# Performance work log

Measured on AMD Instinct MI355X. Metric: run time of the kernel, lower is better.

Reference implementation:

```python
import jax, jax.numpy as jnp
import numpy as np

B, T, C, H, HS, L, V = 16, 2048, 16, 2, 8, 2, 256
EPS = 1e-5


def _ln(x, g, b):
    m = jnp.mean(x, axis=-1, keepdims=True)
    v = jnp.mean((x - m) ** 2, axis=-1, keepdims=True)
    return (x - m) / jnp.sqrt(v + EPS) * g + b


def setup_inputs() -> dict:
    key = jax.random.key(0)
    ks = jax.random.split(key, 10)
    p = lambda k, s: (0.02 * jax.random.normal(k, s)).astype(jnp.float32)
    return {
        "idx": jax.random.randint(ks[0], (B, T), 0, V),
        "tok_emb": p(ks[1], (V, C)),          # tied with lm_head
        "pos_emb": p(ks[2], (T, C)),
        "wq": p(ks[3], (L, H, C, HS)),
        "wk": p(ks[4], (L, H, C, HS)),
        "wv": p(ks[5], (L, H, C, HS)),
        "wo": p(ks[6], (L, C, C)),            # torch Linear weight: (out, in)
        "ln1_g": jnp.ones((L, C), jnp.float32),
        "ln1_b": jnp.zeros((L, C), jnp.float32),
        "ln2_g": jnp.ones((L, C), jnp.float32),
        "ln2_b": jnp.zeros((L, C), jnp.float32),
        "w1": p(ks[7], (L, 4 * C, C)),
        "w2": p(ks[8], (L, C, 4 * C)),
        "lnf_g": jnp.ones((C,), jnp.float32),
        "lnf_b": jnp.zeros((C,), jnp.float32),
    }


def reference(idx, tok_emb, pos_emb, wq, wk, wv, wo, ln1_g, ln1_b,
              ln2_g, ln2_b, w1, w2, lnf_g, lnf_b):
    Tc = idx.shape[1]
    x = tok_emb[idx] + pos_emb[:Tc]                      # [B,T,C]
    causal = jnp.tril(jnp.ones((Tc, Tc), dtype=bool))
    scale = HS ** -0.5
    for l in range(L):
        h = _ln(x, ln1_g[l], ln1_b[l])
        q = jnp.einsum('btc,hcs->bhts', h, wq[l])
        k = jnp.einsum('btc,hcs->bhts', h, wk[l])
        v = jnp.einsum('btc,hcs->bhts', h, wv[l])
        scores = jnp.einsum('bhts,bhus->bhtu', q, k) * scale
        scores = jnp.where(causal, scores, -jnp.inf)
        attn = jax.nn.softmax(scores, axis=-1)           # [B,H,T,T]
        o = jnp.einsum('bhtu,bhus->bhts', attn, v)       # [B,H,T,HS]
        o = o.transpose(0, 2, 1, 3).reshape(x.shape[0], Tc, C)  # concat heads
        x = x + o @ wo[l].T
        h = _ln(x, ln2_g[l], ln2_b[l])
        x = x + jax.nn.relu(h @ w1[l].T) @ w2[l].T
    x = _ln(x, lnf_g, lnf_b)
    return x @ tok_emb.T                                 # tied lm_head: [B,T,V]
```

## Files before the change

kernel.cpp:

```cpp
#include <hip/hip_runtime.h>
#include <math.h>

constexpr int Bc  = 16;
constexpr int Tc  = 2048;
constexpr int Cc  = 16;
constexpr int Hc  = 2;
constexpr int HSc = 8;
constexpr int Vc  = 256;
constexpr int BT  = Bc * Tc;
constexpr float EPSc = 1e-5f;


typedef short s8v __attribute__((ext_vector_type(8)));
typedef float f4v __attribute__((ext_vector_type(4)));

__device__ inline float shx(float v, int m) { return __shfl_xor(v, m, 64); }

__device__ inline unsigned short f2bf(float f) {
  union { float f; unsigned u; } c; c.f = f;
  unsigned u = c.u + 0x7fffu + ((c.u >> 16) & 1u);
  return (unsigned short)(u >> 16);
}

__device__ inline unsigned cvtpk(float a, float b) {
  unsigned r;
  asm("v_cvt_pk_bf16_f32 %0, %1, %2" : "=v"(r) : "v"(a), "v"(b));
  return r;
}

__device__ inline void layernorm16(const float* xr, float* h,
                                   const float* g, const float* b) {
  float m = 0.f;
#pragma unroll
  for (int c = 0; c < Cc; c++) m += xr[c];
  m *= (1.f / Cc);
  float var = 0.f;
#pragma unroll
  for (int c = 0; c < Cc; c++) { float d = xr[c] - m; var += d * d; }
  var *= (1.f / Cc);
  float rs = rsqrtf(var + EPSc);
#pragma unroll
  for (int c = 0; c < Cc; c++) h[c] = (xr[c] - m) * rs * g[c] + b[c];
}

__device__ inline void qkv_store_bf16(const float* h, const float* swq,
                                      const float* swk, const float* swv,
                                      int bb, int tt, int j,
                                      unsigned short* __restrict__ qb,
                                      unsigned short* __restrict__ kb,
                                      unsigned short* sv) {
  const float pre = 0.35355339059327373f * 1.4426950408889634f;
  int a = tt & 31;
  int col = (tt & 32) | ((((a & 15) >> 2)) << 3) | (((a >> 4) & 1) << 2) |
            (a & 3);
#pragma unroll
  for (int hh = 0; hh < Hc; hh++) {
    float q0 = 0.f, q1 = 0.f, k0 = 0.f, k1 = 0.f, v0 = 0.f, v1 = 0.f;
#pragma unroll
    for (int c = 0; c < Cc; c++) {
      float hv = h[c];
      const float* wqp = swq + (hh * Cc + c) * HSc + 2 * j;
      const float* wkp = swk + (hh * Cc + c) * HSc + 2 * j;
      const float* wvp = swv + (hh * Cc + c) * HSc + 2 * j;
      q0 += hv * wqp[0]; q1 += hv * wqp[1];
      k0 += hv * wkp[0]; k1 += hv * wkp[1];
      v0 += hv * wvp[0]; v1 += hv * wvp[1];
    }
    int bh = bb * Hc + hh;
    long rowb = ((long)bh * Tc + tt) * 8 + 2 * j;
    unsigned qp = (unsigned)f2bf(q0 * pre) | ((unsigned)f2bf(q1 * pre) << 16);
    unsigned kp = (unsigned)f2bf(k0) | ((unsigned)f2bf(k1) << 16);
    *(unsigned*)(qb + rowb) = qp;
    *(unsigned*)(kb + rowb) = kp;
    sv[(hh * 8 + 2 * j) * 64 + col]     = f2bf(v0);
    sv[(hh * 8 + 2 * j + 1) * 64 + col] = f2bf(v1);
  }
}

__device__ inline void vt_writeout(const unsigned short* sv, int bb, int t0,
                                   int tid, unsigned short* __restrict__ vt) {
  int r  = tid >> 4;
  int cs = (tid & 15) * 4;
  int bh = bb * Hc + (r >> 3);
  int d  = r & 7;
  *(uint2*)(vt + ((long)bh * 8 + d) * Tc + t0 + cs) =
      *(const uint2*)(sv + r * 64 + cs);
}

__global__ __launch_bounds__(256, 4) void embed_ln_qkv_kernel(
    const int* __restrict__ idx, const float* __restrict__ tok,
    const float* __restrict__ pos,
    const float* __restrict__ wq, const float* __restrict__ wk,
    const float* __restrict__ wv,
    const float* __restrict__ g, const float* __restrict__ b,
    float* __restrict__ x, unsigned short* __restrict__ qb,
    unsigned short* __restrict__ kb, unsigned short* __restrict__ vt,
    unsigned short* __restrict__ zp, unsigned short* __restrict__ tokb) {
  __shared__ float swq[256], swk[256], swv[256], sg[Cc], sb[Cc];
  __shared__ unsigned short sv[16 * 64];
  int tid = threadIdx.x;
  if (blockIdx.x == 0) {
    if (tid < 16) ((unsigned*)zp)[tid] = 0u;
    const float4* tp = (const float4*)(tok + tid * Cc);
    float4 t0 = tp[0], t1 = tp[1], t2 = tp[2], t3 = tp[3];
    unsigned* tb = (unsigned*)(tokb + tid * 16);
    tb[0] = cvtpk(t0.x, t0.y); tb[1] = cvtpk(t0.z, t0.w);
    tb[2] = cvtpk(t1.x, t1.y); tb[3] = cvtpk(t1.z, t1.w);
    tb[4] = cvtpk(t2.x, t2.y); tb[5] = cvtpk(t2.z, t2.w);
    tb[6] = cvtpk(t3.x, t3.y); tb[7] = cvtpk(t3.z, t3.w);
  }
  swq[tid] = wq[tid];
  swk[tid] = wk[tid];
  swv[tid] = wv[tid];
  if (tid < Cc) { sg[tid] = g[tid]; sb[tid] = b[tid]; }
  __syncthreads();

  int tk = blockIdx.x * 64 + (tid >> 2);
  int j  = tid & 3;
  int tt = tk & (Tc - 1);
  int bb = tk >> 11;
  int id = idx[tk];
  float xr[Cc];
  const float4* te = (const float4*)(tok + id * Cc);
  const float4* pe = (const float4*)(pos + tt * Cc);
#pragma unroll
  for (int i = 0; i < 4; i++) {
    float4 a = te[i], p = pe[i];
    xr[4*i] = a.x + p.x; xr[4*i+1] = a.y + p.y;
    xr[4*i+2] = a.z + p.z; xr[4*i+3] = a.w + p.w;
  }
  ((float4*)(x + (long)tk * Cc))[j] =
      make_float4(xr[4*j], xr[4*j+1], xr[4*j+2], xr[4*j+3]);
  float h[Cc];
  layernorm16(xr, h, sg, sb);
  qkv_store_bf16(h, swq, swk, swv, bb, tt, j, qb, kb, sv);
  __syncthreads();
  vt_writeout(sv, bb, (blockIdx.x * 64) & (Tc - 1), tid, vt);
}

__global__ __launch_bounds__(64, 4) void attn_kernel(
    const unsigned short* __restrict__ qb,
    const unsigned short* __restrict__ kb,
    const unsigned short* __restrict__ vt,
    const unsigned short* __restrict__ zp,
    float* __restrict__ o) {
  int pairId = blockIdx.x >> 5;
  int bh     = blockIdx.x & 31;
  int lane   = threadIdx.x;
  int lq     = lane & 15;
  int g4     = (lane >> 4) << 2;
  bool real16 = lane < 16;
  bool real8  = lq < 8;
  bool md[4];
#pragma unroll
  for (int r = 0; r < 4; r++) md[r] = (g4 + r) <= lq;

  const f4v zf = {0.f, 0.f, 0.f, 0.f};

#pragma unroll 1
  for (int hf = 0; hf < 2; hf++) {
    int qt = hf ? (127 - pairId) : pairId;
    int q0 = qt << 4;
    int NB = (qt + 2) >> 1;

    s8v qf = *(real16 ? (const s8v*)(qb + ((long)bh * Tc + q0 + lq) * 8)
                      : (const s8v*)zp);
    const unsigned short* kp_ = real16 ? kb + ((long)bh * Tc + lq) * 8
                                       : zp;
    long kts = real16 ? 128 : 0;
    const unsigned short* vp_ =
        real8 ? vt + ((long)bh * 8 + lq) * Tc + (g4 << 1) : zp;
    long vts = real8 ? 32 : 0;

    f4v oacc = zf;
    float lsum = 0.f;

    s8v kf0 = *(const s8v*)kp_;
    s8v kf1 = *(const s8v*)(kp_ + kts);
    kp_ += 2 * kts;
    s8v vf = *(const s8v*)vp_;
    vp_ += vts;

    for (int b = 0; b < NB - 1; b++) {
      s8v kn0 = *(const s8v*)kp_;
      s8v kn1 = *(const s8v*)(kp_ + kts);
      kp_ += 2 * kts;
      s8v vn = *(const s8v*)vp_;
      vp_ += vts;

      f4v st0 = __builtin_amdgcn_mfma_f32_16x16x32_bf16(kf0, qf, zf, 0, 0, 0);
      f4v st1 = __builtin_amdgcn_mfma_f32_16x16x32_bf16(kf1, qf, zf, 0, 0, 0);
      float p00 = __builtin_amdgcn_exp2f(st0[0]);
      float p01 = __builtin_amdgcn_exp2f(st0[1]);
      float p02 = __builtin_amdgcn_exp2f(st0[2]);
      float p03 = __builtin_amdgcn_exp2f(st0[3]);
      float p10 = __builtin_amdgcn_exp2f(st1[0]);
      float p11 = __builtin_amdgcn_exp2f(st1[1]);
      float p12 = __builtin_amdgcn_exp2f(st1[2]);
      float p13 = __builtin_amdgcn_exp2f(st1[3]);
      lsum += ((p00 + p01) + (p02 + p03)) + ((p10 + p11) + (p12 + p13));
      union { unsigned u[4]; s8v s; } pu;
      pu.u[0] = cvtpk(p00, p01);
      pu.u[1] = cvtpk(p02, p03);
      pu.u[2] = cvtpk(p10, p11);
      pu.u[3] = cvtpk(p12, p13);
      oacc = __builtin_amdgcn_mfma_f32_16x16x32_bf16(pu.s, vf, oacc, 0, 0, 0);
      kf0 = kn0; kf1 = kn1; vf = vn;
    }

    {
      f4v st0 = __builtin_amdgcn_mfma_f32_16x16x32_bf16(kf0, qf, zf, 0, 0, 0);
      float p0[4], p1[4];
#pragma unroll
      for (int r = 0; r < 4; r++) p0[r] = __builtin_amdgcn_exp2f(st0[r]);
      if (qt & 1) {
        f4v st1 = __builtin_amdgcn_mfma_f32_16x16x32_bf16(kf1, qf, zf, 0, 0, 0);
#pragma unroll
        for (int r = 0; r < 4; r++) {
          float e = __builtin_amdgcn_exp2f(st1[r]);
          p1[r] = md[r] ? e : 0.f;
        }
      } else {
#pragma unroll
        for (int r = 0; r < 4; r++) {
          p0[r] = md[r] ? p0[r] : 0.f;
          p1[r] = 0.f;
        }
      }
      lsum += ((p0[0] + p0[1]) + (p0[2] + p0[3])) +
              ((p1[0] + p1[1]) + (p1[2] + p1[3]));
      union { unsigned u[4]; s8v s; } pu;
      pu.u[0] = cvtpk(p0[0], p0[1]);
      pu.u[1] = cvtpk(p0[2], p0[3]);
      pu.u[2] = cvtpk(p1[0], p1[1]);
      pu.u[3] = cvtpk(p1[2], p1[3]);
      oacc = __builtin_amdgcn_mfma_f32_16x16x32_bf16(pu.s, vf, oacc, 0, 0, 0);
    }

    lsum += shx(lsum, 16);
    lsum += shx(lsum, 32);
    float inv = 1.0f / lsum;
    float invr[4];
#pragma unroll
    for (int r = 0; r < 4; r++) invr[r] = __shfl(inv, g4 + r, 64);
    if (real8) {
      float* ob = o + ((long)bh * Tc + q0 + g4) * 8 + lq;
#pragma unroll
      for (int r = 0; r < 4; r++) ob[r * 8] = oacc[r] * invr[r];
    }
  }
}

__device__ inline void coop_tail(
    const float* __restrict__ o,
    const float* swo, const float* sw1, const float* sw2,
    const float* sg2, const float* sb2, int bb, int tt, int j, float* xr) {
  int hh = j & 1;
  int bh = bb * Hc + hh;
  const float4* op = (const float4*)(o + ((long)bh * Tc + tt) * 8);
  float4 a = op[0], b = op[1];
  float own[8] = {a.x, a.y, a.z, a.w, b.x, b.y, b.z, b.w};
  float oth[8];
#pragma unroll
  for (int s = 0; s < 8; s++) oth[s] = shx(own[s], 1);
  float orow[Cc];
#pragma unroll
  for (int s = 0; s < 8; s++) {
    orow[s]     = (hh == 0) ? own[s] : oth[s];
    orow[8 + s] = (hh == 0) ? oth[s] : own[s];
  }
  float xc[4];
#pragma unroll
  for (int qq = 0; qq < 4; qq++) {
    int c = 4 * j + qq;
    float acc = xr[c];
#pragma unroll
    for (int kk = 0; kk < Cc; kk++) acc += orow[kk] * swo[c * 17 + kk];
    xc[qq] = acc;
  }
  {
    float p[4];
#pragma unroll
    for (int qq = 0; qq < 4; qq++) p[qq] = shx(xc[qq], 1);
    bool lo = (j & 1) == 0;
    float a8[8], b8[8];
#pragma unroll
    for (int qq = 0; qq < 4; qq++) {
      a8[qq]     = lo ? xc[qq] : p[qq];
      a8[4 + qq] = lo ? p[qq] : xc[qq];
    }
#pragma unroll
    for (int s = 0; s < 8; s++) b8[s] = shx(a8[s], 2);
    bool lo2 = (j & 2) == 0;
#pragma unroll
    for (int s = 0; s < 8; s++) {
      xr[s]     = lo2 ? a8[s] : b8[s];
      xr[8 + s] = lo2 ? b8[s] : a8[s];
    }
  }
  float h[Cc];
  layernorm16(xr, h, sg2, sb2);
  float r[Cc];
#pragma unroll
  for (int c = 0; c < Cc; c++) r[c] = 0.f;
#pragma unroll
  for (int i = 0; i < 16; i++) {
    int jj = j * 16 + i;
    float acc = 0.f;
#pragma unroll
    for (int c = 0; c < Cc; c++) acc += h[c] * sw1[jj * 17 + c];
    acc = fmaxf(acc, 0.f);
#pragma unroll
    for (int c = 0; c < Cc; c++) r[c] += acc * sw2[c * 64 + jj];
  }
#pragma unroll
  for (int c = 0; c < Cc; c++) r[c] += shx(r[c], 1);
#pragma unroll
  for (int c = 0; c < Cc; c++) r[c] += shx(r[c], 2);
#pragma unroll
  for (int c = 0; c < Cc; c++) xr[c] += r[c];
}

__global__ __launch_bounds__(256, 4) void red_mid_kernel(
    const float* __restrict__ o,
    const float* __restrict__ wo, const float* __restrict__ g2,
    const float* __restrict__ b2, const float* __restrict__ w1,
    const float* __restrict__ w2,
    const float* __restrict__ wq, const float* __restrict__ wk,
    const float* __restrict__ wv, const float* __restrict__ g1,
    const float* __restrict__ b1,
    float* __restrict__ x, unsigned short* __restrict__ qb,
    unsigned short* __restrict__ kb, unsigned short* __restrict__ vt) {
  __shared__ float swo[16 * 17], sw1[64 * 17], sw2[1024];
  __shared__ float swq[256], swk[256], swv[256];
  __shared__ float sg2[Cc], sb2[Cc], sg1[Cc], sb1[Cc];
  __shared__ unsigned short sv[16 * 64];
  int tid = threadIdx.x;
  swq[tid] = wq[tid]; swk[tid] = wk[tid]; swv[tid] = wv[tid];
  { int rr = tid >> 4, c = tid & 15; swo[rr * 17 + c] = wo[tid]; }
#pragma unroll
  for (int t = tid; t < 1024; t += 256) {
    int jj = t >> 4, c = t & 15;
    sw1[jj * 17 + c] = w1[t];
    sw2[t] = w2[t];
  }
  if (tid < Cc) {
    sg2[tid] = g2[tid]; sb2[tid] = b2[tid];
    sg1[tid] = g1[tid]; sb1[tid] = b1[tid];
  }
  __syncthreads();

  int tk = blockIdx.x * 64 + (tid >> 2);
  int j  = tid & 3;
  int bb = tk >> 11, tt = tk & (Tc - 1);
  float xr[Cc];
  const float4* xp = (const float4*)(x + (long)tk * Cc);
#pragma unroll
  for (int i = 0; i < 4; i++) {
    float4 a = xp[i];
    xr[4*i]=a.x; xr[4*i+1]=a.y; xr[4*i+2]=a.z; xr[4*i+3]=a.w;
  }
  coop_tail(o, swo, sw1, sw2, sg2, sb2, bb, tt, j, xr);
  ((float4*)(x + (long)tk * Cc))[j] =
      make_float4(xr[4*j], xr[4*j+1], xr[4*j+2], xr[4*j+3]);
  float h[Cc];
  layernorm16(xr, h, sg1, sb1);
  qkv_store_bf16(h, swq, swk, swv, bb, tt, j, qb, kb, sv);
  __syncthreads();
  vt_writeout(sv, bb, (blockIdx.x * 64) & (Tc - 1), tid, vt);
}

__global__ __launch_bounds__(256, 4) void red_lnf_head_kernel(
    const float* __restrict__ o,
    const float* __restrict__ wo, const float* __restrict__ g2,
    const float* __restrict__ b2, const float* __restrict__ w1,
    const float* __restrict__ w2, const float* __restrict__ gf,
    const float* __restrict__ bf,
    const float* __restrict__ x, const unsigned short* __restrict__ tokb,
    const unsigned short* __restrict__ zp, float* __restrict__ out) {
  __shared__ float swo[16 * 17], sw1[64 * 17], sw2[1024];
  __shared__ float sg2[Cc], sb2[Cc], sgf[Cc], sbf[Cc];
  __shared__ unsigned short shb[64 * 16];
  int tid = threadIdx.x;
  { int rr = tid >> 4, c = tid & 15; swo[rr * 17 + c] = wo[tid]; }
#pragma unroll
  for (int t = tid; t < 1024; t += 256) {
    int jj = t >> 4, c = t & 15;
    sw1[jj * 17 + c] = w1[t];
    sw2[t] = w2[t];
  }
  if (tid < Cc) {
    sg2[tid] = g2[tid]; sb2[tid] = b2[tid];
    sgf[tid] = gf[tid]; sbf[tid] = bf[tid];
  }
  __syncthreads();

  int tk = blockIdx.x * 64 + (tid >> 2);
  int j  = tid & 3;
  int bb = tk >> 11, tt = tk & (Tc - 1);
  float xr[Cc];
  const float4* xp = (const float4*)(x + (long)tk * Cc);
#pragma unroll
  for (int i = 0; i < 4; i++) {
    float4 a = xp[i];
    xr[4*i]=a.x; xr[4*i+1]=a.y; xr[4*i+2]=a.z; xr[4*i+3]=a.w;
  }
  coop_tail(o, swo, sw1, sw2, sg2, sb2, bb, tt, j, xr);
  float h[Cc];
  layernorm16(xr, h, sgf, sbf);
  *(uint2*)(shb + (tid >> 2) * 16 + 4 * j) =
      make_uint2(cvtpk(h[4*j], h[4*j+1]), cvtpk(h[4*j+2], h[4*j+3]));
  __syncthreads();

  int wv = tid >> 6;
  int l  = tid & 63;
  int lg = l >> 4;
  bool realg = lg < 2;
  s8v hb = realg
      ? *(const s8v*)(shb + (wv * 16 + (l & 15)) * 16 + 8 * lg)
      : *(const s8v*)zp;
  const unsigned short* abase = realg ? tokb + (l & 15) * 16 + 8 * lg : zp;
  long astep = realg ? 256 : 0;
  const f4v zf = {0.f, 0.f, 0.f, 0.f};
  long trow = (long)(blockIdx.x * 64 + wv * 16 + (l & 15)) * Vc;
  int vbase = 4 * lg;
#pragma unroll 4
  for (int n = 0; n < 16; n++) {
    s8v af = *(const s8v*)(abase + n * astep);
    f4v d = __builtin_amdgcn_mfma_f32_16x16x32_bf16(af, hb, zf, 0, 0, 0);
    *(float4*)(out + trow + n * 16 + vbase) =
        make_float4(d[0], d[1], d[2], d[3]);
  }
}

extern "C" void kernel_launch(void* const* d_in, const int* in_sizes, int n_in,
                              void* d_out, int out_size, void* d_ws,
                              size_t ws_size, hipStream_t stream) {
  const int*   idx  = (const int*)  d_in[0];
  const float* tok  = (const float*)d_in[1];
  const float* pos  = (const float*)d_in[2];
  const float* wq   = (const float*)d_in[3];
  const float* wk   = (const float*)d_in[4];
  const float* wv   = (const float*)d_in[5];
  const float* wo   = (const float*)d_in[6];
  const float* ln1g = (const float*)d_in[7];
  const float* ln1b = (const float*)d_in[8];
  const float* ln2g = (const float*)d_in[9];
  const float* ln2b = (const float*)d_in[10];
  const float* w1   = (const float*)d_in[11];
  const float* w2   = (const float*)d_in[12];
  const float* lnfg = (const float*)d_in[13];
  const float* lnfb = (const float*)d_in[14];
  float* out = (float*)d_out;

  float* x = (float*)d_ws;
  float* o = x + (long)BT * Cc;
  unsigned short* qb = (unsigned short*)(o + (long)Bc * Hc * Tc * HSc);
  unsigned short* kb = qb + (long)Bc * Hc * Tc * HSc;
  unsigned short* vt = kb + (long)Bc * Hc * Tc * HSc;
  unsigned short* tokb = vt + (long)Bc * Hc * Tc * HSc;
  unsigned short* zp = tokb + Vc * Cc;

  embed_ln_qkv_kernel<<<BT / 64, 256, 0, stream>>>(
      idx, tok, pos, wq, wk, wv, ln1g, ln1b, x, qb, kb, vt, zp, tokb);
  attn_kernel<<<2048, 64, 0, stream>>>(qb, kb, vt, zp, o);
  red_mid_kernel<<<BT / 64, 256, 0, stream>>>(
      o, wo, ln2g, ln2b, w1, w2,
      wq + Hc * Cc * HSc, wk + Hc * Cc * HSc, wv + Hc * Cc * HSc,
      ln1g + Cc, ln1b + Cc, x, qb, kb, vt);
  attn_kernel<<<2048, 64, 0, stream>>>(qb, kb, vt, zp, o);
  red_lnf_head_kernel<<<BT / 64, 256, 0, stream>>>(
      o, wo + Cc * Cc, ln2g + Cc, ln2b + Cc,
      w1 + 4 * Cc * Cc, w2 + 4 * Cc * Cc, lnfg, lnfb, x, tokb, zp, out);
}
```

Baseline: 170.3 us.

## Fuse attention with the following MLP/QKV tail kernels via shared-memory handoff

Attention is now computed inside the per-layer tail kernel. Each 128-thread block handles both heads for one causal-balanced pair of query tiles and hands the attention output to the Wo/MLP/LN/QKV (or LN-final/lm_head) stage through shared memory instead of a global 'o' buffer. This removes two kernel launches and the global round trip of the attention output. Because the next layer's QKV is written while other blocks still read the current one, QKV/V^T buffers are double-buffered per layer. The trade-off is small 128-thread blocks that each reload all weights into LDS, and the attention phase's causal imbalance is now coupled with the tail work.

```diff
diff --git a/kernel.cpp b/kernel.cpp
--- a/kernel.cpp
+++ b/kernel.cpp
@@ -138,17 +138,14 @@
   vt_writeout(sv, bb, (blockIdx.x * 64) & (Tc - 1), tid, vt);
 }
 
-__global__ __launch_bounds__(64, 4) void attn_kernel(
-    const unsigned short* __restrict__ qb,
-    const unsigned short* __restrict__ kb,
-    const unsigned short* __restrict__ vt,
-    const unsigned short* __restrict__ zp,
-    float* __restrict__ o) {
-  int pairId = blockIdx.x >> 5;
-  int bh     = blockIdx.x & 31;
-  int lane   = threadIdx.x;
-  int lq     = lane & 15;
-  int g4     = (lane >> 4) << 2;
+__device__ inline void attn_wave(const unsigned short* __restrict__ qb,
+                                 const unsigned short* __restrict__ kb,
+                                 const unsigned short* __restrict__ vt,
+                                 const unsigned short* __restrict__ zp,
+                                 int bh, int pairId, int lane, int wv_,
+                                 float* so) {
+  int lq = lane & 15;
+  int g4 = (lane >> 4) << 2;
   bool real16 = lane < 16;
   bool real8  = lq < 8;
   bool md[4];
@@ -165,8 +162,7 @@
 
     s8v qf = *(real16 ? (const s8v*)(qb + ((long)bh * Tc + q0 + lq) * 8)
                       : (const s8v*)zp);
-    const unsigned short* kp_ = real16 ? kb + ((long)bh * Tc + lq) * 8
-                                       : zp;
+    const unsigned short* kp_ = real16 ? kb + ((long)bh * Tc + lq) * 8 : zp;
     long kts = real16 ? 128 : 0;
     const unsigned short* vp_ =
         real8 ? vt + ((long)bh * 8 + lq) * Tc + (g4 << 1) : zp;
@@ -214,7 +210,8 @@
 #pragma unroll
       for (int r = 0; r < 4; r++) p0[r] = __builtin_amdgcn_exp2f(st0[r]);
       if (qt & 1) {
-        f4v st1 = __builtin_amdgcn_mfma_f32_16x16x32_bf16(kf1, qf, zf, 0, 0, 0);
+        f4v st1 =
+            __builtin_amdgcn_mfma_f32_16x16x32_bf16(kf1, qf, zf, 0, 0, 0);
 #pragma unroll
         for (int r = 0; r < 4; r++) {
           float e = __builtin_amdgcn_exp2f(st1[r]);
@@ -244,30 +241,24 @@
 #pragma unroll
     for (int r = 0; r < 4; r++) invr[r] = __shfl(inv, g4 + r, 64);
     if (real8) {
-      float* ob = o + ((long)bh * Tc + q0 + g4) * 8 + lq;
-#pragma unroll
-      for (int r = 0; r < 4; r++) ob[r * 8] = oacc[r] * invr[r];
-    }
-  }
-}
-
-__device__ inline void coop_tail(
-    const float* __restrict__ o,
-    const float* swo, const float* sw1, const float* sw2,
-    const float* sg2, const float* sb2, int bb, int tt, int j, float* xr) {
-  int hh = j & 1;
-  int bh = bb * Hc + hh;
-  const float4* op = (const float4*)(o + ((long)bh * Tc + tt) * 8);
-  float4 a = op[0], b = op[1];
-  float own[8] = {a.x, a.y, a.z, a.w, b.x, b.y, b.z, b.w};
-  float oth[8];
-#pragma unroll
-  for (int s = 0; s < 8; s++) oth[s] = shx(own[s], 1);
+      float* ob = so + (hf * 16 + g4) * Cc + wv_ * 8 + lq;
+#pragma unroll
+      for (int r = 0; r < 4; r++) ob[r * Cc] = oacc[r] * invr[r];
+    }
+  }
+}
+
+__device__ inline void tail_core(
+    const float* so, const float* swo, const float* sw1, const float* sw2,
+    const float* sg2, const float* sb2, int tl, int j, float* xr) {
   float orow[Cc];
-#pragma unroll
-  for (int s = 0; s < 8; s++) {
-    orow[s]     = (hh == 0) ? own[s] : oth[s];
-    orow[8 + s] = (hh == 0) ? oth[s] : own[s];
+  {
+    const float4* op = (const float4*)(so + tl * Cc);
+    float4 a = op[0], b = op[1], c = op[2], d = op[3];
+    orow[0]=a.x; orow[1]=a.y; orow[2]=a.z; orow[3]=a.w;
+    orow[4]=b.x; orow[5]=b.y; orow[6]=b.z; orow[7]=b.w;
+    orow[8]=c.x; orow[9]=c.y; orow[10]=c.z; orow[11]=c.w;
+    orow[12]=d.x; orow[13]=d.y; orow[14]=d.z; orow[15]=d.w;
   }
   float xc[4];
 #pragma unroll
@@ -321,27 +312,31 @@
   for (int c = 0; c < Cc; c++) xr[c] += r[c];
 }
 
-__global__ __launch_bounds__(256, 4) void red_mid_kernel(
-    const float* __restrict__ o,
+__global__ __launch_bounds__(128, 2) void attn_mid_kernel(
+    const unsigned short* __restrict__ qb0,
+    const unsigned short* __restrict__ kb0,
+    const unsigned short* __restrict__ vt0,
+    const unsigned short* __restrict__ zp,
     const float* __restrict__ wo, const float* __restrict__ g2,
     const float* __restrict__ b2, const float* __restrict__ w1,
     const float* __restrict__ w2,
     const float* __restrict__ wq, const float* __restrict__ wk,
     const float* __restrict__ wv, const float* __restrict__ g1,
     const float* __restrict__ b1,
-    float* __restrict__ x, unsigned short* __restrict__ qb,
-    unsigned short* __restrict__ kb, unsigned short* __restrict__ vt) {
+    float* __restrict__ x, unsigned short* __restrict__ qb1,
+    unsigned short* __restrict__ kb1, unsigned short* __restrict__ vt1) {
   __shared__ float swo[16 * 17], sw1[64 * 17], sw2[1024];
   __shared__ float swq[256], swk[256], swv[256];
   __shared__ float sg2[Cc], sb2[Cc], sg1[Cc], sb1[Cc];
-  __shared__ unsigned short sv[16 * 64];
+  __shared__ float so[32 * Cc];
+  __shared__ unsigned short sv[2 * 16 * 16];
   int tid = threadIdx.x;
-  swq[tid] = wq[tid]; swk[tid] = wk[tid]; swv[tid] = wv[tid];
-  { int rr = tid >> 4, c = tid & 15; swo[rr * 17 + c] = wo[tid]; }
-#pragma unroll
-  for (int t = tid; t < 1024; t += 256) {
-    int jj = t >> 4, c = t & 15;
-    sw1[jj * 17 + c] = w1[t];
+  for (int t = tid; t < 256; t += 128) {
+    swq[t] = wq[t]; swk[t] = wk[t]; swv[t] = wv[t];
+    swo[(t >> 4) * 17 + (t & 15)] = wo[t];
+  }
+  for (int t = tid; t < 1024; t += 128) {
+    sw1[(t >> 4) * 17 + (t & 15)] = w1[t];
     sw2[t] = w2[t];
   }
   if (tid < Cc) {
@@ -350,43 +345,90 @@
   }
   __syncthreads();
 
-  int tk = blockIdx.x * 64 + (tid >> 2);
-  int j  = tid & 3;
-  int bb = tk >> 11, tt = tk & (Tc - 1);
+  int b  = blockIdx.x & 15;
+  int p  = blockIdx.x >> 4;
+  int wv_ = tid >> 6, lane = tid & 63;
+  attn_wave(qb0, kb0, vt0, zp, b * Hc + wv_, p, lane, wv_, so);
+  __syncthreads();
+
+  int tl = tid >> 2, j = tid & 3;
+  int qtT = (tl < 16) ? p : (127 - p);
+  int tt  = qtT * 16 + (tl & 15);
+  long tk = (long)b * Tc + tt;
   float xr[Cc];
-  const float4* xp = (const float4*)(x + (long)tk * Cc);
-#pragma unroll
-  for (int i = 0; i < 4; i++) {
-    float4 a = xp[i];
-    xr[4*i]=a.x; xr[4*i+1]=a.y; xr[4*i+2]=a.z; xr[4*i+3]=a.w;
-  }
-  coop_tail(o, swo, sw1, sw2, sg2, sb2, bb, tt, j, xr);
-  ((float4*)(x + (long)tk * Cc))[j] =
+  {
+    const float4* xp = (const float4*)(x + tk * Cc);
+#pragma unroll
+    for (int i = 0; i < 4; i++) {
+      float4 a = xp[i];
+      xr[4*i]=a.x; xr[4*i+1]=a.y; xr[4*i+2]=a.z; xr[4*i+3]=a.w;
+    }
+  }
+  tail_core(so, swo, sw1, sw2, sg2, sb2, tl, j, xr);
+  ((float4*)(x + tk * Cc))[j] =
       make_float4(xr[4*j], xr[4*j+1], xr[4*j+2], xr[4*j+3]);
   float h[Cc];
   layernorm16(xr, h, sg1, sb1);
-  qkv_store_bf16(h, swq, swk, swv, bb, tt, j, qb, kb, sv);
-  __syncthreads();
-  vt_writeout(sv, bb, (blockIdx.x * 64) & (Tc - 1), tid, vt);
-}
-
-__global__ __launch_bounds__(256, 4) void red_lnf_head_kernel(
-    const float* __restrict__ o,
+  {
+    const float pre = 0.35355339059327373f * 1.4426950408889634f;
+    int i  = tt & 15;
+    int cd = 4 * (i >> 2) + (i & 3);
+    int tau = tl >> 4;
+#pragma unroll
+    for (int hh = 0; hh < Hc; hh++) {
+      float q0 = 0.f, q1 = 0.f, k0 = 0.f, k1 = 0.f, v0 = 0.f, v1 = 0.f;
+#pragma unroll
+      for (int c = 0; c < Cc; c++) {
+        float hv = h[c];
+        const float* wqp = swq + (hh * Cc + c) * HSc + 2 * j;
+        const float* wkp = swk + (hh * Cc + c) * HSc + 2 * j;
+        const float* wvp = swv + (hh * Cc + c) * HSc + 2 * j;
+        q0 += hv * wqp[0]; q1 += hv * wqp[1];
+        k0 += hv * wkp[0]; k1 += hv * wkp[1];
+        v0 += hv * wvp[0]; v1 += hv * wvp[1];
+      }
+      int bh = b * Hc + hh;
+      long rowb = ((long)bh * Tc + tt) * 8 + 2 * j;
+      *(unsigned*)(qb1 + rowb) =
+          (unsigned)f2bf(q0 * pre) | ((unsigned)f2bf(q1 * pre) << 16);
+      *(unsigned*)(kb1 + rowb) =
+          (unsigned)f2bf(k0) | ((unsigned)f2bf(k1) << 16);
+      sv[(tau * 16 + hh * 8 + 2 * j) * 16 + cd]     = f2bf(v0);
+      sv[(tau * 16 + hh * 8 + 2 * j + 1) * 16 + cd] = f2bf(v1);
+    }
+  }
+  __syncthreads();
+  {
+    int tau = tid >> 6, rr = (tid >> 2) & 15, G = tid & 3;
+    int qt_ = tau ? (127 - p) : p;
+    int bh  = b * Hc + (rr >> 3), d = rr & 7;
+    int gcol = ((qt_ & ~1) << 4) + 8 * G + 4 * (qt_ & 1);
+    *(uint2*)(vt1 + ((long)bh * 8 + d) * Tc + gcol) =
+        *(const uint2*)(sv + (tau * 16 + rr) * 16 + 4 * G);
+  }
+}
+
+__global__ __launch_bounds__(128, 2) void attn_lnf_head_kernel(
+    const unsigned short* __restrict__ qb1,
+    const unsigned short* __restrict__ kb1,
+    const unsigned short* __restrict__ vt1,
+    const unsigned short* __restrict__ zp,
     const float* __restrict__ wo, const float* __restrict__ g2,
     const float* __restrict__ b2, const float* __restrict__ w1,
     const float* __restrict__ w2, const float* __restrict__ gf,
     const float* __restrict__ bf,
-    const float* __restrict__ x, const unsigned short* __restrict__ tokb,
-    const unsigned short* __restrict__ zp, float* __restrict__ out) {
+    float* __restrict__ x, const unsigned short* __restrict__ tokb,
+    float* __restrict__ out) {
   __shared__ float swo[16 * 17], sw1[64 * 17], sw2[1024];
   __shared__ float sg2[Cc], sb2[Cc], sgf[Cc], sbf[Cc];
-  __shared__ unsigned short shb[64 * 16];
+  __shared__ float so[32 * Cc];
+  __shared__ unsigned short shb[32 * 16];
   int tid = threadIdx.x;
-  { int rr = tid >> 4, c = tid & 15; swo[rr * 17 + c] = wo[tid]; }
-#pragma unroll
-  for (int t = tid; t < 1024; t += 256) {
-    int jj = t >> 4, c = t & 15;
-    sw1[jj * 17 + c] = w1[t];
+  for (int t = tid; t < 256; t += 128) {
+    swo[(t >> 4) * 17 + (t & 15)] = wo[t];
+  }
+  for (int t = tid; t < 1024; t += 128) {
+    sw1[(t >> 4) * 17 + (t & 15)] = w1[t];
     sw2[t] = w2[t];
   }
   if (tid < Cc) {
@@ -395,34 +437,44 @@
   }
   __syncthreads();
 
-  int tk = blockIdx.x * 64 + (tid >> 2);
-  int j  = tid & 3;
-  int bb = tk >> 11, tt = tk & (Tc - 1);
+  int b  = blockIdx.x & 15;
+  int p  = blockIdx.x >> 4;
+  int wv_ = tid >> 6, lane = tid & 63;
+  attn_wave(qb1, kb1, vt1, zp, b * Hc + wv_, p, lane, wv_, so);
+  __syncthreads();
+
+  int tl = tid >> 2, j = tid & 3;
+  int qtT = (tl < 16) ? p : (127 - p);
+  int tt  = qtT * 16 + (tl & 15);
+  long tk = (long)b * Tc + tt;
   float xr[Cc];
-  const float4* xp = (const float4*)(x + (long)tk * Cc);
-#pragma unroll
-  for (int i = 0; i < 4; i++) {
-    float4 a = xp[i];
-    xr[4*i]=a.x; xr[4*i+1]=a.y; xr[4*i+2]=a.z; xr[4*i+3]=a.w;
-  }
-  coop_tail(o, swo, sw1, sw2, sg2, sb2, bb, tt, j, xr);
+  {
+    const float4* xp = (const float4*)(x + tk * Cc);
+#pragma unroll
+    for (int i = 0; i < 4; i++) {
+      float4 a = xp[i];
+      xr[4*i]=a.x; xr[4*i+1]=a.y; xr[4*i+2]=a.z; xr[4*i+3]=a.w;
+    }
+  }
+  tail_core(so, swo, sw1, sw2, sg2, sb2, tl, j, xr);
   float h[Cc];
   layernorm16(xr, h, sgf, sbf);
-  *(uint2*)(shb + (tid >> 2) * 16 + 4 * j) =
+  *(uint2*)(shb + tl * 16 + 4 * j) =
       make_uint2(cvtpk(h[4*j], h[4*j+1]), cvtpk(h[4*j+2], h[4*j+3]));
   __syncthreads();
 
-  int wv = tid >> 6;
   int l  = tid & 63;
   int lg = l >> 4;
   bool realg = lg < 2;
+  int wv2 = tid >> 6;
   s8v hb = realg
-      ? *(const s8v*)(shb + (wv * 16 + (l & 15)) * 16 + 8 * lg)
+      ? *(const s8v*)(shb + (wv2 * 16 + (l & 15)) * 16 + 8 * lg)
       : *(const s8v*)zp;
   const unsigned short* abase = realg ? tokb + (l & 15) * 16 + 8 * lg : zp;
   long astep = realg ? 256 : 0;
   const f4v zf = {0.f, 0.f, 0.f, 0.f};
-  long trow = (long)(blockIdx.x * 64 + wv * 16 + (l & 15)) * Vc;
+  int qtH = wv2 ? (127 - p) : p;
+  long trow = ((long)b * Tc + qtH * 16 + (l & 15)) * Vc;
   int vbase = 4 * lg;
 #pragma unroll 4
   for (int n = 0; n < 16; n++) {
@@ -454,22 +506,22 @@
   float* out = (float*)d_out;
 
   float* x = (float*)d_ws;
-  float* o = x + (long)BT * Cc;
-  unsigned short* qb = (unsigned short*)(o + (long)Bc * Hc * Tc * HSc);
-  unsigned short* kb = qb + (long)Bc * Hc * Tc * HSc;
-  unsigned short* vt = kb + (long)Bc * Hc * Tc * HSc;
-  unsigned short* tokb = vt + (long)Bc * Hc * Tc * HSc;
-  unsigned short* zp = tokb + Vc * Cc;
+  unsigned short* qb0 = (unsigned short*)(x + (long)BT * Cc);
+  unsigned short* kb0 = qb0 + (long)Bc * Hc * Tc * HSc;
+  unsigned short* vt0 = kb0 + (long)Bc * Hc * Tc * HSc;
+  unsigned short* qb1 = vt0 + (long)Bc * Hc * Tc * HSc;
+  unsigned short* kb1 = qb1 + (long)Bc * Hc * Tc * HSc;
+  unsigned short* vt1 = kb1 + (long)Bc * Hc * Tc * HSc;
+  unsigned short* tokb = vt1 + (long)Bc * Hc * Tc * HSc;
+  unsigned short* zp   = tokb + Vc * Cc;
 
   embed_ln_qkv_kernel<<<BT / 64, 256, 0, stream>>>(
-      idx, tok, pos, wq, wk, wv, ln1g, ln1b, x, qb, kb, vt, zp, tokb);
-  attn_kernel<<<2048, 64, 0, stream>>>(qb, kb, vt, zp, o);
-  red_mid_kernel<<<BT / 64, 256, 0, stream>>>(
-      o, wo, ln2g, ln2b, w1, w2,
+      idx, tok, pos, wq, wk, wv, ln1g, ln1b, x, qb0, kb0, vt0, zp, tokb);
+  attn_mid_kernel<<<1024, 128, 0, stream>>>(
+      qb0, kb0, vt0, zp, wo, ln2g, ln2b, w1, w2,
       wq + Hc * Cc * HSc, wk + Hc * Cc * HSc, wv + Hc * Cc * HSc,
-      ln1g + Cc, ln1b + Cc, x, qb, kb, vt);
-  attn_kernel<<<2048, 64, 0, stream>>>(qb, kb, vt, zp, o);
-  red_lnf_head_kernel<<<BT / 64, 256, 0, stream>>>(
-      o, wo + Cc * Cc, ln2g + Cc, ln2b + Cc,
-      w1 + 4 * Cc * Cc, w2 + 4 * Cc * Cc, lnfg, lnfb, x, tokb, zp, out);
-}
+      ln1g + Cc, ln1b + Cc, x, qb1, kb1, vt1);
+  attn_lnf_head_kernel<<<1024, 128, 0, stream>>>(
+      qb1, kb1, vt1, zp, wo + Cc * Cc, ln2g + Cc, ln2b + Cc,
+      w1 + 4 * Cc * Cc, w2 + 4 * Cc * Cc, lnfg, lnfb, x, tokb, out);
+}
```

Measured after the change: 167.2 us. Within noise of the previous version (-1.8%).
